# Optimization experiments

Measured on AMD Instinct MI355X. Metric: run time of the kernel, lower is better.

The kernel has to match this reference:

```python
import jax, jax.numpy as jnp
import numpy as np

B, N, C = 32, 512, 768
H = 12
D = C // H
HID = 4 * C
EPS = 1e-5


def layer_norm(x, w, b):
    mu = jnp.mean(x, axis=-1, keepdims=True)
    var = jnp.mean(jnp.square(x - mu), axis=-1, keepdims=True)
    return (x - mu) * jax.lax.rsqrt(var + EPS) * w + b


def setup_inputs() -> dict:
    key = jax.random.key(0)
    ks = jax.random.split(key, 8)
    s_in = 1.0 / np.sqrt(C)
    s_hid = 1.0 / np.sqrt(HID)
    return {
        "x": jax.random.normal(ks[0], (B, N, C), dtype=jnp.float32),
        "ln1_w": jnp.ones((C,), jnp.float32),
        "ln1_b": jnp.zeros((C,), jnp.float32),
        "qkv_w": jax.random.normal(ks[1], (3 * C, C), jnp.float32) * s_in,
        "proj_w": jax.random.normal(ks[2], (C, C), jnp.float32) * s_in,
        "proj_b": jnp.zeros((C,), jnp.float32),
        "ln2_w": jnp.ones((C,), jnp.float32),
        "ln2_b": jnp.zeros((C,), jnp.float32),
        "fc1_w": jax.random.normal(ks[3], (HID, C), jnp.float32) * s_in,
        "fc1_b": jnp.zeros((HID,), jnp.float32),
        "fc2_w": jax.random.normal(ks[4], (C, HID), jnp.float32) * s_hid,
        "fc2_b": jnp.zeros((C,), jnp.float32),
    }


def reference(x, ln1_w, ln1_b, qkv_w, proj_w, proj_b, ln2_w, ln2_b, fc1_w, fc1_b, fc2_w, fc2_b):
    scale = D ** (-0.5)
    # --- attention on norm1(x) ---
    h = layer_norm(x, ln1_w, ln1_b)                       # [B,N,C]
    qkv = jnp.einsum('bnc,fc->bnf', h, qkv_w)             # [B,N,3C] (no bias)
    qkv = qkv.reshape(B, N, 3, H, D).transpose(2, 0, 3, 1, 4)  # [3,B,H,N,D]
    q, k, v = qkv[0], qkv[1], qkv[2]
    attn = jnp.einsum('bhnd,bhmd->bhnm', q, k) * scale    # [B,H,N,N]
    attn = jax.nn.softmax(attn, axis=-1)
    o = jnp.einsum('bhnm,bhmd->bhnd', attn, v)            # [B,H,N,D]
    o = o.transpose(0, 2, 1, 3).reshape(B, N, C)
    o = jnp.einsum('bnc,oc->bno', o, proj_w) + proj_b
    # --- Block quirk: x = attn_out + drop_path(attn_out) == 2*attn_out (eval) ---
    x = o + o
    # --- MLP residual ---
    h2 = layer_norm(x, ln2_w, ln2_b)
    h2 = jnp.einsum('bnc,hc->bnh', h2, fc1_w) + fc1_b
    h2 = jax.nn.gelu(h2, approximate=False)
    h2 = jnp.einsum('bnh,oh->bno', h2, fc2_w) + fc2_b
    return x + h2
```

## Files before the change

### kernel.cpp

```cpp
#include <hip/hip_runtime.h>

#define B_   32
#define N_   512
#define C_   768
#define H_   12
#define D_   64
#define HID_ 3072
#define BN_  (B_*N_)

typedef unsigned short u16;
typedef __attribute__((ext_vector_type(8))) short  short8;
typedef __attribute__((ext_vector_type(4))) float  float4v;

__device__ __forceinline__ u16 f32_to_bf16(float f) {
  unsigned u = __builtin_bit_cast(unsigned, f);
  u += 0x7fffu + ((u >> 16) & 1u);
  return (u16)(u >> 16);
}

__device__ __forceinline__ void load_lds16(const u16* g, u16* l) {
  __builtin_amdgcn_global_load_lds(
      (const __attribute__((address_space(1))) unsigned int*)g,
      (__attribute__((address_space(3))) unsigned int*)l,
      16, 0, 0);
}

__global__ void cast_kernel(const float* __restrict__ src, u16* __restrict__ dst, int n) {
  int i = blockIdx.x * 256 + threadIdx.x;
  if (i < n) dst[i] = f32_to_bf16(src[i]);
}

__global__ __launch_bounds__(256)
void ln_kernel(const float* __restrict__ x, const float* __restrict__ w,
               const float* __restrict__ bias, u16* __restrict__ out) {
  const int row = blockIdx.x;
  const int tid = threadIdx.x;
  const float* xr = x + (size_t)row * C_;
  float v0 = xr[tid], v1 = xr[tid + 256], v2 = xr[tid + 512];
  float s = v0 + v1 + v2;
  float q = v0*v0 + v1*v1 + v2*v2;
#pragma unroll
  for (int off = 1; off < 64; off <<= 1) { s += __shfl_xor(s, off); q += __shfl_xor(q, off); }
  __shared__ float red[8];
  int wave = tid >> 6, lane = tid & 63;
  if (lane == 0) { red[wave] = s; red[4 + wave] = q; }
  __syncthreads();
  s = red[0] + red[1] + red[2] + red[3];
  q = red[4] + red[5] + red[6] + red[7];
  float mean = s * (1.0f / C_);
  float var  = q * (1.0f / C_) - mean * mean;
  float rstd = rsqrtf(var + 1e-5f);
  u16* orow = out + (size_t)row * C_;
  orow[tid]       = f32_to_bf16((v0 - mean) * rstd * w[tid]       + bias[tid]);
  orow[tid + 256] = f32_to_bf16((v1 - mean) * rstd * w[tid + 256] + bias[tid + 256]);
  orow[tid + 512] = f32_to_bf16((v2 - mean) * rstd * w[tid + 512] + bias[tid + 512]);
}

template <int EPI>
__device__ __forceinline__ void gemm_core(const u16* __restrict__ A, const u16* __restrict__ W,
                                          int N, int K,
                                          const float* __restrict__ bias,
                                          const float* __restrict__ resid,
                                          u16* __restrict__ out_bf, float* __restrict__ out_f) {
  __shared__ alignas(16) u16 As[128 * 64];
  __shared__ alignas(16) u16 Ws[128 * 64];
  const int tid  = threadIdx.x;
  const int wave = tid >> 6;
  const int lane = tid & 63;
  const int quad = lane >> 4;
  const int l15  = lane & 15;

  const int nx    = gridDim.x;
  const int lin   = blockIdx.y * nx + blockIdx.x;
  const int total = nx * gridDim.y;
  const int v     = (lin & 7) * (total >> 3) + (lin >> 3);
  const int m0 = (v / nx) << 7;
  const int n0 = (v % nx) << 7;

  const int wm = (wave >> 1) * 64;
  const int wn = (wave & 1) * 64;

  float4v acc[4][4];
#pragma unroll
  for (int i = 0; i < 4; i++)
#pragma unroll
    for (int j = 0; j < 4; j++) acc[i][j] = (float4v){0.f, 0.f, 0.f, 0.f};

  const int c0   = wave * 4;
  const int srow = lane >> 3;
  const int gcol = ((lane & 7) ^ srow) * 8;
  const u16* Ag[4];
  const u16* Wg[4];
#pragma unroll
  for (int j = 0; j < 4; j++) {
    const int row = (c0 + j) * 8 + srow;
    Ag[j] = A + (size_t)(m0 + row) * K + gcol;
    Wg[j] = W + (size_t)(n0 + row) * K + gcol;
  }

  for (int k0 = 0; k0 < K; k0 += 64) {
    __syncthreads();
#pragma unroll
    for (int j = 0; j < 4; j++) load_lds16(Ag[j] + k0, &As[(c0 + j) * 512]);
#pragma unroll
    for (int j = 0; j < 4; j++) load_lds16(Wg[j] + k0, &Ws[(c0 + j) * 512]);
    __syncthreads();

    short8 af[4][2], bf[4][2];
#pragma unroll
    for (int mi = 0; mi < 4; mi++)
#pragma unroll
      for (int ks = 0; ks < 2; ks++) {
        const int swz = ((ks * 4 + quad) ^ (l15 & 7)) * 8;
        af[mi][ks] = *(const short8*)&As[(wm + mi * 16 + l15) * 64 + swz];
        bf[mi][ks] = *(const short8*)&Ws[(wn + mi * 16 + l15) * 64 + swz];
      }
#pragma unroll
    for (int ks = 0; ks < 2; ks++)
#pragma unroll
      for (int mi = 0; mi < 4; mi++)
#pragma unroll
        for (int ni = 0; ni < 4; ni++)
          acc[mi][ni] = __builtin_amdgcn_mfma_f32_16x16x32_bf16(af[mi][ks], bf[ni][ks], acc[mi][ni], 0, 0, 0);
  }

#pragma unroll
  for (int mi = 0; mi < 4; mi++) {
#pragma unroll
    for (int r = 0; r < 4; r++) {
      const int row = m0 + wm + mi * 16 + quad * 4 + r;
#pragma unroll
      for (int ni = 0; ni < 4; ni++) {
        const int col = n0 + wn + ni * 16 + l15;
        float v2 = acc[mi][ni][r];
        if (EPI == 0) {
          out_bf[(size_t)row * N + col] = f32_to_bf16(v2);
        } else if (EPI == 1) {
          v2 += bias[col];
          v2 = 0.5f * v2 * (1.0f + erff(v2 * 0.70710678118654752f));
          out_bf[(size_t)row * N + col] = f32_to_bf16(v2);
        } else if (EPI == 2) {
          out_f[(size_t)row * N + col] = 2.0f * (v2 + bias[col]);
        } else {
          out_f[(size_t)row * N + col] = v2 + bias[col] + resid[(size_t)row * N + col];
        }
      }
    }
  }
}

__global__ __launch_bounds__(256, 3)
void gemm_qkv(const u16* __restrict__ A, const u16* __restrict__ W, int N, int K,
              u16* __restrict__ out_bf) {
  gemm_core<0>(A, W, N, K, nullptr, nullptr, out_bf, nullptr);
}
__global__ __launch_bounds__(256, 3)
void gemm_proj2x(const u16* __restrict__ A, const u16* __restrict__ W, int N, int K,
                 const float* __restrict__ bias, float* __restrict__ out_f) {
  gemm_core<2>(A, W, N, K, bias, nullptr, nullptr, out_f);
}
__global__ __launch_bounds__(256, 3)
void gemm_fc1gelu(const u16* __restrict__ A, const u16* __restrict__ W, int N, int K,
                  const float* __restrict__ bias, u16* __restrict__ out_bf) {
  gemm_core<1>(A, W, N, K, bias, nullptr, out_bf, nullptr);
}
__global__ __launch_bounds__(256, 3)
void gemm_fc2res(const u16* __restrict__ A, const u16* __restrict__ W, int N, int K,
                 const float* __restrict__ bias, const float* __restrict__ resid,
                 float* __restrict__ out_f) {
  gemm_core<3>(A, W, N, K, bias, resid, nullptr, out_f);
}

__global__ __launch_bounds__(256)
void attn_kernel(const u16* __restrict__ qkv, u16* __restrict__ o) {
  __shared__ alignas(16) u16 Ks[64 * 64];
  __shared__ alignas(16) u16 Vt[64 * 64];
  __shared__ alignas(16) u16 Ps[4][16 * 64];
  const int tid  = threadIdx.x;
  const int wave = tid >> 6, lane = tid & 63;
  const int quad = lane >> 4, l15 = lane & 15;
  const int qt = blockIdx.x, h = blockIdx.y, b = blockIdx.z;
  const size_t rs3 = 3 * C_;

  const int qrow = b * N_ + qt * 64 + wave * 16 + l15;
  const u16* qp = qkv + (size_t)qrow * rs3 + h * D_ + quad * 8;
  const short8 qf0 = *(const short8*)qp;
  const short8 qf1 = *(const short8*)(qp + 32);

  float m[4], l[4];
  float4v oacc[4];
#pragma unroll
  for (int r = 0; r < 4; r++) { m[r] = -1e30f; l[r] = 0.f; }
#pragma unroll
  for (int ni = 0; ni < 4; ni++) oacc[ni] = (float4v){0.f, 0.f, 0.f, 0.f};

  const int vkey = tid >> 2, vdg = tid & 3;

  for (int kt = 0; kt < 8; ++kt) {
    __syncthreads();
    {
      int c0 = wave * 2, c1 = c0 + 1;
      int kr0 = c0 * 8 + (lane >> 3), kr1 = c1 * 8 + (lane >> 3);
      int kc = (lane & 7) * 8;
      const u16* kg = qkv + (size_t)(b * N_ + kt * 64) * rs3 + C_ + h * D_;
      load_lds16(kg + (size_t)kr0 * rs3 + kc, &Ks[c0 * 512]);
      load_lds16(kg + (size_t)kr1 * rs3 + kc, &Ks[c1 * 512]);
    }
    {
      const u16* vg = qkv + (size_t)(b * N_ + kt * 64 + vkey) * rs3 + 2 * C_ + h * D_ + vdg * 16;
      short8 v0 = *(const short8*)vg;
      short8 v1 = *(const short8*)(vg + 8);
#pragma unroll
      for (int j = 0; j < 8; j++) Vt[(vdg * 16 + j) * 64 + vkey] = (u16)v0[j];
#pragma unroll
      for (int j = 0; j < 8; j++) Vt[(vdg * 16 + 8 + j) * 64 + vkey] = (u16)v1[j];
    }
    __syncthreads();

    float4v s[4];
#pragma unroll
    for (int ni = 0; ni < 4; ni++) {
      s[ni] = (float4v){0.f, 0.f, 0.f, 0.f};
      short8 kf0 = *(const short8*)&Ks[(ni * 16 + l15) * 64 + quad * 8];
      short8 kf1 = *(const short8*)&Ks[(ni * 16 + l15) * 64 + 32 + quad * 8];
      s[ni] = __builtin_amdgcn_mfma_f32_16x16x32_bf16(qf0, kf0, s[ni], 0, 0, 0);
      s[ni] = __builtin_amdgcn_mfma_f32_16x16x32_bf16(qf1, kf1, s[ni], 0, 0, 0);
    }

    float mt[4];
#pragma unroll
    for (int r = 0; r < 4; r++)
      mt[r] = 0.125f * fmaxf(fmaxf(s[0][r], s[1][r]), fmaxf(s[2][r], s[3][r]));
#pragma unroll
    for (int off = 1; off < 16; off <<= 1)
#pragma unroll
      for (int r = 0; r < 4; r++) mt[r] = fmaxf(mt[r], __shfl_xor(mt[r], off));

    float alpha[4], mnew[4], rsum[4];
#pragma unroll
    for (int r = 0; r < 4; r++) {
      mnew[r] = fmaxf(m[r], mt[r]);
      alpha[r] = __expf(m[r] - mnew[r]);
      rsum[r] = 0.f;
    }
#pragma unroll
    for (int ni = 0; ni < 4; ni++)
#pragma unroll
      for (int r = 0; r < 4; r++) {
        float p = __expf(s[ni][r] * 0.125f - mnew[r]);
        rsum[r] += p;
        Ps[wave][(quad * 4 + r) * 64 + ni * 16 + l15] = f32_to_bf16(p);
      }
#pragma unroll
    for (int off = 1; off < 16; off <<= 1)
#pragma unroll
      for (int r = 0; r < 4; r++) rsum[r] += __shfl_xor(rsum[r], off);
#pragma unroll
    for (int r = 0; r < 4; r++) { l[r] = l[r] * alpha[r] + rsum[r]; m[r] = mnew[r]; }
#pragma unroll
    for (int ni = 0; ni < 4; ni++)
#pragma unroll
      for (int r = 0; r < 4; r++) oacc[ni][r] *= alpha[r];

    __syncthreads();

#pragma unroll
    for (int ks = 0; ks < 2; ks++) {
      short8 pf = *(const short8*)&Ps[wave][l15 * 64 + ks * 32 + quad * 8];
#pragma unroll
      for (int ni = 0; ni < 4; ni++) {
        short8 vf = *(const short8*)&Vt[(ni * 16 + l15) * 64 + ks * 32 + quad * 8];
        oacc[ni] = __builtin_amdgcn_mfma_f32_16x16x32_bf16(pf, vf, oacc[ni], 0, 0, 0);
      }
    }
  }

#pragma unroll
  for (int ni = 0; ni < 4; ni++)
#pragma unroll
    for (int r = 0; r < 4; r++) {
      int row = b * N_ + qt * 64 + wave * 16 + quad * 4 + r;
      int col = h * D_ + ni * 16 + l15;
      o[(size_t)row * C_ + col] = f32_to_bf16(oacc[ni][r] / l[r]);
    }
}

extern "C" void kernel_launch(void* const* d_in, const int* in_sizes, int n_in,
                              void* d_out, int out_size, void* d_ws, size_t ws_size,
                              hipStream_t stream) {
  const float* x      = (const float*)d_in[0];
  const float* ln1_w  = (const float*)d_in[1];
  const float* ln1_b  = (const float*)d_in[2];
  const float* qkv_w  = (const float*)d_in[3];
  const float* proj_w = (const float*)d_in[4];
  const float* proj_b = (const float*)d_in[5];
  const float* ln2_w  = (const float*)d_in[6];
  const float* ln2_b  = (const float*)d_in[7];
  const float* fc1_w  = (const float*)d_in[8];
  const float* fc1_b  = (const float*)d_in[9];
  const float* fc2_w  = (const float*)d_in[10];
  const float* fc2_b  = (const float*)d_in[11];
  float* out = (float*)d_out;

  char* ws = (char*)d_ws;
  size_t off = 0;
  auto alloc = [&](size_t bytes) { void* p = ws + off; off += (bytes + 255) & ~255ull; return p; };
  u16* wqkv  = (u16*)alloc((size_t)3 * C_ * C_ * 2);
  u16* wproj = (u16*)alloc((size_t)C_ * C_ * 2);
  u16* wfc1  = (u16*)alloc((size_t)HID_ * C_ * 2);
  u16* wfc2  = (u16*)alloc((size_t)C_ * HID_ * 2);
  u16* regionA = (u16*)alloc((size_t)BN_ * HID_ * 2);
  float* xnew  = (float*)alloc((size_t)BN_ * C_ * 4);
  u16* h2      = (u16*)alloc((size_t)BN_ * C_ * 2);

  u16* hbuf = regionA;
  u16* qkvb = regionA + (size_t)BN_ * C_;
  u16* obuf = regionA;
  u16* act  = regionA;

  cast_kernel<<<dim3(3 * C_ * C_ / 256), 256, 0, stream>>>(qkv_w, wqkv, 3 * C_ * C_);
  cast_kernel<<<dim3(C_ * C_ / 256), 256, 0, stream>>>(proj_w, wproj, C_ * C_);
  cast_kernel<<<dim3(HID_ * C_ / 256), 256, 0, stream>>>(fc1_w, wfc1, HID_ * C_);
  cast_kernel<<<dim3(HID_ * C_ / 256), 256, 0, stream>>>(fc2_w, wfc2, C_ * HID_);

  ln_kernel<<<dim3(BN_), 256, 0, stream>>>(x, ln1_w, ln1_b, hbuf);

  gemm_qkv<<<dim3(3 * C_ / 128, BN_ / 128), 256, 0, stream>>>(hbuf, wqkv, 3 * C_, C_, qkvb);

  attn_kernel<<<dim3(N_ / 64, H_, B_), 256, 0, stream>>>(qkvb, obuf);

  gemm_proj2x<<<dim3(C_ / 128, BN_ / 128), 256, 0, stream>>>(obuf, wproj, C_, C_, proj_b, xnew);

  ln_kernel<<<dim3(BN_), 256, 0, stream>>>(xnew, ln2_w, ln2_b, h2);

  gemm_fc1gelu<<<dim3(HID_ / 128, BN_ / 128), 256, 0, stream>>>(h2, wfc1, HID_, C_, fc1_b, act);

  gemm_fc2res<<<dim3(C_ / 128, BN_ / 128), 256, 0, stream>>>(act, wfc2, C_, HID_, fc2_b, xnew, out);
}
```

Baseline: 573.7 us.

## Write V transposed from QKV GEMM and read K/V directly in attention

The QKV GEMM epilogue now writes the V columns in a per-head transposed [B,H,D,N] layout into a reused workspace buffer. The attention kernel drops the shared-memory staging of K and V and loads MFMA fragments straight from global memory, which also removes the block-wide barriers. The per-wave P tile gets an XOR swizzle against bank conflicts, and the final division becomes a reciprocal multiply. In exchange, the V stores in the GEMM are scattered and uncoalesced, and every wave now reads K/V from global memory or cache without reuse through LDS.

```diff
diff --git a/kernel.cpp b/kernel.cpp
--- a/kernel.cpp
+++ b/kernel.cpp
@@ -61,7 +61,8 @@
                                           int N, int K,
                                           const float* __restrict__ bias,
                                           const float* __restrict__ resid,
-                                          u16* __restrict__ out_bf, float* __restrict__ out_f) {
+                                          u16* __restrict__ out_bf, float* __restrict__ out_f,
+                                          u16* __restrict__ vt_out) {
   __shared__ alignas(16) u16 As[128 * 64];
   __shared__ alignas(16) u16 Ws[128 * 64];
   const int tid  = threadIdx.x;
@@ -134,7 +135,14 @@
         const int col = n0 + wn + ni * 16 + l15;
         float v2 = acc[mi][ni][r];
         if (EPI == 0) {
-          out_bf[(size_t)row * N + col] = f32_to_bf16(v2);
+          if (col < 2 * C_) {
+            out_bf[(size_t)row * N + col] = f32_to_bf16(v2);
+          } else {
+            const int voff = col - 2 * C_;
+            const int hh = voff >> 6, dd = voff & 63;
+            const int bb = row >> 9, nn = row & 511;
+            vt_out[((size_t)(bb * H_ + hh) * D_ + dd) * N_ + nn] = f32_to_bf16(v2);
+          }
         } else if (EPI == 1) {
           v2 += bias[col];
           v2 = 0.5f * v2 * (1.0f + erff(v2 * 0.70710678118654752f));
@@ -151,42 +159,45 @@
 
 __global__ __launch_bounds__(256, 3)
 void gemm_qkv(const u16* __restrict__ A, const u16* __restrict__ W, int N, int K,
-              u16* __restrict__ out_bf) {
-  gemm_core<0>(A, W, N, K, nullptr, nullptr, out_bf, nullptr);
+              u16* __restrict__ out_bf, u16* __restrict__ vt_out) {
+  gemm_core<0>(A, W, N, K, nullptr, nullptr, out_bf, nullptr, vt_out);
 }
 __global__ __launch_bounds__(256, 3)
 void gemm_proj2x(const u16* __restrict__ A, const u16* __restrict__ W, int N, int K,
                  const float* __restrict__ bias, float* __restrict__ out_f) {
-  gemm_core<2>(A, W, N, K, bias, nullptr, nullptr, out_f);
+  gemm_core<2>(A, W, N, K, bias, nullptr, nullptr, out_f, nullptr);
 }
 __global__ __launch_bounds__(256, 3)
 void gemm_fc1gelu(const u16* __restrict__ A, const u16* __restrict__ W, int N, int K,
                   const float* __restrict__ bias, u16* __restrict__ out_bf) {
-  gemm_core<1>(A, W, N, K, bias, nullptr, out_bf, nullptr);
+  gemm_core<1>(A, W, N, K, bias, nullptr, out_bf, nullptr, nullptr);
 }
 __global__ __launch_bounds__(256, 3)
 void gemm_fc2res(const u16* __restrict__ A, const u16* __restrict__ W, int N, int K,
                  const float* __restrict__ bias, const float* __restrict__ resid,
                  float* __restrict__ out_f) {
-  gemm_core<3>(A, W, N, K, bias, resid, nullptr, out_f);
+  gemm_core<3>(A, W, N, K, bias, resid, nullptr, out_f, nullptr);
 }
 
 __global__ __launch_bounds__(256)
-void attn_kernel(const u16* __restrict__ qkv, u16* __restrict__ o) {
-  __shared__ alignas(16) u16 Ks[64 * 64];
-  __shared__ alignas(16) u16 Vt[64 * 64];
+void attn_kernel(const u16* __restrict__ qkv, const u16* __restrict__ vt,
+                 u16* __restrict__ o) {
   __shared__ alignas(16) u16 Ps[4][16 * 64];
   const int tid  = threadIdx.x;
   const int wave = tid >> 6, lane = tid & 63;
   const int quad = lane >> 4, l15 = lane & 15;
   const int qt = blockIdx.x, h = blockIdx.y, b = blockIdx.z;
   const size_t rs3 = 3 * C_;
+  u16* myPs = Ps[wave];
 
   const int qrow = b * N_ + qt * 64 + wave * 16 + l15;
   const u16* qp = qkv + (size_t)qrow * rs3 + h * D_ + quad * 8;
   const short8 qf0 = *(const short8*)qp;
   const short8 qf1 = *(const short8*)(qp + 32);
 
+  const u16* kbase = qkv + (size_t)(b * N_) * rs3 + C_ + h * D_ + quad * 8;
+  const u16* vbase = vt + (size_t)(b * H_ + h) * D_ * N_ + quad * 8;
+
   float m[4], l[4];
   float4v oacc[4];
 #pragma unroll
@@ -194,35 +205,14 @@
 #pragma unroll
   for (int ni = 0; ni < 4; ni++) oacc[ni] = (float4v){0.f, 0.f, 0.f, 0.f};
 
-  const int vkey = tid >> 2, vdg = tid & 3;
-
   for (int kt = 0; kt < 8; ++kt) {
-    __syncthreads();
-    {
-      int c0 = wave * 2, c1 = c0 + 1;
-      int kr0 = c0 * 8 + (lane >> 3), kr1 = c1 * 8 + (lane >> 3);
-      int kc = (lane & 7) * 8;
-      const u16* kg = qkv + (size_t)(b * N_ + kt * 64) * rs3 + C_ + h * D_;
-      load_lds16(kg + (size_t)kr0 * rs3 + kc, &Ks[c0 * 512]);
-      load_lds16(kg + (size_t)kr1 * rs3 + kc, &Ks[c1 * 512]);
-    }
-    {
-      const u16* vg = qkv + (size_t)(b * N_ + kt * 64 + vkey) * rs3 + 2 * C_ + h * D_ + vdg * 16;
-      short8 v0 = *(const short8*)vg;
-      short8 v1 = *(const short8*)(vg + 8);
-#pragma unroll
-      for (int j = 0; j < 8; j++) Vt[(vdg * 16 + j) * 64 + vkey] = (u16)v0[j];
-#pragma unroll
-      for (int j = 0; j < 8; j++) Vt[(vdg * 16 + 8 + j) * 64 + vkey] = (u16)v1[j];
-    }
-    __syncthreads();
-
     float4v s[4];
 #pragma unroll
     for (int ni = 0; ni < 4; ni++) {
+      const u16* kr = kbase + (size_t)(kt * 64 + ni * 16 + l15) * rs3;
+      short8 kf0 = *(const short8*)kr;
+      short8 kf1 = *(const short8*)(kr + 32);
       s[ni] = (float4v){0.f, 0.f, 0.f, 0.f};
-      short8 kf0 = *(const short8*)&Ks[(ni * 16 + l15) * 64 + quad * 8];
-      short8 kf1 = *(const short8*)&Ks[(ni * 16 + l15) * 64 + 32 + quad * 8];
       s[ni] = __builtin_amdgcn_mfma_f32_16x16x32_bf16(qf0, kf0, s[ni], 0, 0, 0);
       s[ni] = __builtin_amdgcn_mfma_f32_16x16x32_bf16(qf1, kf1, s[ni], 0, 0, 0);
     }
@@ -249,7 +239,9 @@
       for (int r = 0; r < 4; r++) {
         float p = __expf(s[ni][r] * 0.125f - mnew[r]);
         rsum[r] += p;
-        Ps[wave][(quad * 4 + r) * 64 + ni * 16 + l15] = f32_to_bf16(p);
+        const int prow = quad * 4 + r;
+        const int g = (ni * 2 + (l15 >> 3)) ^ (prow & 7);
+        myPs[prow * 64 + g * 8 + (l15 & 7)] = f32_to_bf16(p);
       }
 #pragma unroll
     for (int off = 1; off < 16; off <<= 1)
@@ -262,26 +254,29 @@
 #pragma unroll
       for (int r = 0; r < 4; r++) oacc[ni][r] *= alpha[r];
 
-    __syncthreads();
-
 #pragma unroll
     for (int ks = 0; ks < 2; ks++) {
-      short8 pf = *(const short8*)&Ps[wave][l15 * 64 + ks * 32 + quad * 8];
+      const int g = (ks * 4 + quad) ^ (l15 & 7);
+      short8 pf = *(const short8*)&myPs[l15 * 64 + g * 8];
 #pragma unroll
       for (int ni = 0; ni < 4; ni++) {
-        short8 vf = *(const short8*)&Vt[(ni * 16 + l15) * 64 + ks * 32 + quad * 8];
+        const u16* vr = vbase + (size_t)(ni * 16 + l15) * N_ + kt * 64 + ks * 32;
+        short8 vf = *(const short8*)vr;
         oacc[ni] = __builtin_amdgcn_mfma_f32_16x16x32_bf16(pf, vf, oacc[ni], 0, 0, 0);
       }
     }
   }
 
+  float inv[4];
+#pragma unroll
+  for (int r = 0; r < 4; r++) inv[r] = 1.0f / l[r];
 #pragma unroll
   for (int ni = 0; ni < 4; ni++)
 #pragma unroll
     for (int r = 0; r < 4; r++) {
       int row = b * N_ + qt * 64 + wave * 16 + quad * 4 + r;
       int col = h * D_ + ni * 16 + l15;
-      o[(size_t)row * C_ + col] = f32_to_bf16(oacc[ni][r] / l[r]);
+      o[(size_t)row * C_ + col] = f32_to_bf16(oacc[ni][r] * inv[r]);
     }
 }
 
@@ -317,6 +312,7 @@
   u16* qkvb = regionA + (size_t)BN_ * C_;
   u16* obuf = regionA;
   u16* act  = regionA;
+  u16* vtbuf = (u16*)xnew;
 
   cast_kernel<<<dim3(3 * C_ * C_ / 256), 256, 0, stream>>>(qkv_w, wqkv, 3 * C_ * C_);
   cast_kernel<<<dim3(C_ * C_ / 256), 256, 0, stream>>>(proj_w, wproj, C_ * C_);
@@ -325,9 +321,9 @@
 
   ln_kernel<<<dim3(BN_), 256, 0, stream>>>(x, ln1_w, ln1_b, hbuf);
 
-  gemm_qkv<<<dim3(3 * C_ / 128, BN_ / 128), 256, 0, stream>>>(hbuf, wqkv, 3 * C_, C_, qkvb);
-
-  attn_kernel<<<dim3(N_ / 64, H_, B_), 256, 0, stream>>>(qkvb, obuf);
+  gemm_qkv<<<dim3(3 * C_ / 128, BN_ / 128), 256, 0, stream>>>(hbuf, wqkv, 3 * C_, C_, qkvb, vtbuf);
+
+  attn_kernel<<<dim3(N_ / 64, H_, B_), 256, 0, stream>>>(qkvb, vtbuf, obuf);
 
   gemm_proj2x<<<dim3(C_ / 128, BN_ / 128), 256, 0, stream>>>(obuf, wproj, C_, C_, proj_b, xnew);
 
```

After: 666.1 us. +16.1%, slower.

## Pre-transpose V and process two query tiles per attention block with swizzled LDS

Applied to the files above, without the earlier changes.

Adds a separate kernel that transposes V into a per-head [D,N] buffer, reusing the xnew scratch region, so the attention kernel can stream both K and V into LDS with async global-to-LDS loads instead of a scalar transposing scatter. Each attention block now handles 128 queries, two 64-row subtiles per wave, so every K/V tile loaded is reused twice, and the grid is linearised with the query tile as the slow index. K, V and P in LDS use an XOR swizzle to avoid bank conflicts, and the barrier between the softmax and the PV product is removed because each wave owns its P buffer. This costs an extra kernel launch plus a round trip of V through memory, and roughly doubles the register state per thread.

```diff
diff --git a/kernel.cpp b/kernel.cpp
--- a/kernel.cpp
+++ b/kernel.cpp
@@ -56,6 +56,28 @@
   orow[tid + 512] = f32_to_bf16((v2 - mean) * rstd * w[tid + 512] + bias[tid + 512]);
 }
 
+__global__ __launch_bounds__(256)
+void transpose_v(const u16* __restrict__ qkv, u16* __restrict__ vt) {
+  __shared__ alignas(16) u16 T[64 * 72];
+  const int nt = blockIdx.x, bh = blockIdx.y;
+  const int b = bh / H_, h = bh % H_;
+  const int tid = threadIdx.x;
+  const size_t rs3 = 3 * C_;
+  const int r = tid >> 2, dc = (tid & 3) * 16;
+  const u16* src = qkv + (size_t)(b * N_ + nt * 64 + r) * rs3 + 2 * C_ + h * D_ + dc;
+  short8 a0 = *(const short8*)src;
+  short8 a1 = *(const short8*)(src + 8);
+#pragma unroll
+  for (int j = 0; j < 8; j++) T[(dc + j) * 72 + r] = (u16)a0[j];
+#pragma unroll
+  for (int j = 0; j < 8; j++) T[(dc + 8 + j) * 72 + r] = (u16)a1[j];
+  __syncthreads();
+  const int d = tid >> 2, nc = (tid & 3) * 16;
+  u16* dst = vt + ((size_t)(b * H_ + h) * D_ + d) * N_ + nt * 64 + nc;
+  *(short8*)dst       = *(const short8*)&T[d * 72 + nc];
+  *(short8*)(dst + 8) = *(const short8*)&T[d * 72 + nc + 8];
+}
+
 template <int EPI>
 __device__ __forceinline__ void gemm_core(const u16* __restrict__ A, const u16* __restrict__ W,
                                           int N, int K,
@@ -172,117 +194,137 @@
 }
 
 __global__ __launch_bounds__(256)
-void attn_kernel(const u16* __restrict__ qkv, u16* __restrict__ o) {
+void attn_kernel(const u16* __restrict__ qkv, const u16* __restrict__ vt,
+                 u16* __restrict__ o) {
   __shared__ alignas(16) u16 Ks[64 * 64];
-  __shared__ alignas(16) u16 Vt[64 * 64];
-  __shared__ alignas(16) u16 Ps[4][16 * 64];
+  __shared__ alignas(16) u16 Vs[64 * 64];
+  __shared__ alignas(16) u16 Ps[8][16 * 64];
   const int tid  = threadIdx.x;
   const int wave = tid >> 6, lane = tid & 63;
   const int quad = lane >> 4, l15 = lane & 15;
-  const int qt = blockIdx.x, h = blockIdx.y, b = blockIdx.z;
+  const int lin = blockIdx.x;
+  const int bh = lin % 384, qt = lin / 384;
+  const int b = bh / H_, h = bh % H_;
   const size_t rs3 = 3 * C_;
 
-  const int qrow = b * N_ + qt * 64 + wave * 16 + l15;
-  const u16* qp = qkv + (size_t)qrow * rs3 + h * D_ + quad * 8;
-  const short8 qf0 = *(const short8*)qp;
-  const short8 qf1 = *(const short8*)(qp + 32);
-
-  float m[4], l[4];
-  float4v oacc[4];
-#pragma unroll
-  for (int r = 0; r < 4; r++) { m[r] = -1e30f; l[r] = 0.f; }
-#pragma unroll
-  for (int ni = 0; ni < 4; ni++) oacc[ni] = (float4v){0.f, 0.f, 0.f, 0.f};
-
-  const int vkey = tid >> 2, vdg = tid & 3;
+  short8 qf[2][2];
+#pragma unroll
+  for (int st = 0; st < 2; st++) {
+    const int qrow = b * N_ + qt * 128 + st * 64 + wave * 16 + l15;
+    const u16* qp = qkv + (size_t)qrow * rs3 + h * D_ + quad * 8;
+    qf[st][0] = *(const short8*)qp;
+    qf[st][1] = *(const short8*)(qp + 32);
+  }
+
+  const int srow = lane >> 3;
+  const int gcol = ((lane & 7) ^ srow) * 8;
+  const int ch0 = wave * 2, ch1 = wave * 2 + 1;
+  const u16* kg0 = qkv + (size_t)(b * N_ + ch0 * 8 + srow) * rs3 + C_ + h * D_ + gcol;
+  const u16* kg1 = qkv + (size_t)(b * N_ + ch1 * 8 + srow) * rs3 + C_ + h * D_ + gcol;
+  const u16* vg0 = vt + ((size_t)bh * D_ + ch0 * 8 + srow) * N_ + gcol;
+  const u16* vg1 = vt + ((size_t)bh * D_ + ch1 * 8 + srow) * N_ + gcol;
+
+  float m[2][4], l[2][4];
+  float4v oacc[2][4];
+#pragma unroll
+  for (int st = 0; st < 2; st++)
+#pragma unroll
+    for (int r = 0; r < 4; r++) { m[st][r] = -1e30f; l[st][r] = 0.f; }
+#pragma unroll
+  for (int st = 0; st < 2; st++)
+#pragma unroll
+    for (int ni = 0; ni < 4; ni++) oacc[st][ni] = (float4v){0.f, 0.f, 0.f, 0.f};
 
   for (int kt = 0; kt < 8; ++kt) {
     __syncthreads();
-    {
-      int c0 = wave * 2, c1 = c0 + 1;
-      int kr0 = c0 * 8 + (lane >> 3), kr1 = c1 * 8 + (lane >> 3);
-      int kc = (lane & 7) * 8;
-      const u16* kg = qkv + (size_t)(b * N_ + kt * 64) * rs3 + C_ + h * D_;
-      load_lds16(kg + (size_t)kr0 * rs3 + kc, &Ks[c0 * 512]);
-      load_lds16(kg + (size_t)kr1 * rs3 + kc, &Ks[c1 * 512]);
+    load_lds16(kg0 + (size_t)(kt * 64) * rs3, &Ks[ch0 * 512]);
+    load_lds16(kg1 + (size_t)(kt * 64) * rs3, &Ks[ch1 * 512]);
+    load_lds16(vg0 + kt * 64, &Vs[ch0 * 512]);
+    load_lds16(vg1 + kt * 64, &Vs[ch1 * 512]);
+    __syncthreads();
+
+    short8 kf[4][2];
+#pragma unroll
+    for (int ni = 0; ni < 4; ni++)
+#pragma unroll
+      for (int ks = 0; ks < 2; ks++)
+        kf[ni][ks] = *(const short8*)&Ks[(ni * 16 + l15) * 64 + ((ks * 4 + quad) ^ (l15 & 7)) * 8];
+
+#pragma unroll
+    for (int st = 0; st < 2; st++) {
+      u16* myPs = Ps[wave * 2 + st];
+      float4v s[4];
+#pragma unroll
+      for (int ni = 0; ni < 4; ni++) {
+        s[ni] = (float4v){0.f, 0.f, 0.f, 0.f};
+        s[ni] = __builtin_amdgcn_mfma_f32_16x16x32_bf16(qf[st][0], kf[ni][0], s[ni], 0, 0, 0);
+        s[ni] = __builtin_amdgcn_mfma_f32_16x16x32_bf16(qf[st][1], kf[ni][1], s[ni], 0, 0, 0);
+      }
+
+      float mt[4];
+#pragma unroll
+      for (int r = 0; r < 4; r++)
+        mt[r] = 0.125f * fmaxf(fmaxf(s[0][r], s[1][r]), fmaxf(s[2][r], s[3][r]));
+#pragma unroll
+      for (int off = 1; off < 16; off <<= 1)
+#pragma unroll
+        for (int r = 0; r < 4; r++) mt[r] = fmaxf(mt[r], __shfl_xor(mt[r], off));
+
+      float alpha[4], mnew[4], rsum[4];
+#pragma unroll
+      for (int r = 0; r < 4; r++) {
+        mnew[r] = fmaxf(m[st][r], mt[r]);
+        alpha[r] = __expf(m[st][r] - mnew[r]);
+        rsum[r] = 0.f;
+      }
+#pragma unroll
+      for (int ni = 0; ni < 4; ni++)
+#pragma unroll
+        for (int r = 0; r < 4; r++) {
+          float p = __expf(s[ni][r] * 0.125f - mnew[r]);
+          rsum[r] += p;
+          const int prow = quad * 4 + r;
+          const int g = (ni * 2 + (l15 >> 3)) ^ (prow & 7);
+          myPs[prow * 64 + g * 8 + (l15 & 7)] = f32_to_bf16(p);
+        }
+#pragma unroll
+      for (int off = 1; off < 16; off <<= 1)
+#pragma unroll
+        for (int r = 0; r < 4; r++) rsum[r] += __shfl_xor(rsum[r], off);
+#pragma unroll
+      for (int r = 0; r < 4; r++) { l[st][r] = l[st][r] * alpha[r] + rsum[r]; m[st][r] = mnew[r]; }
+#pragma unroll
+      for (int ni = 0; ni < 4; ni++)
+#pragma unroll
+        for (int r = 0; r < 4; r++) oacc[st][ni][r] *= alpha[r];
+
+#pragma unroll
+      for (int ks = 0; ks < 2; ks++) {
+        const int g = (ks * 4 + quad) ^ (l15 & 7);
+        short8 pf = *(const short8*)&myPs[l15 * 64 + g * 8];
+#pragma unroll
+        for (int ni = 0; ni < 4; ni++) {
+          short8 vf = *(const short8*)&Vs[(ni * 16 + l15) * 64 + ((ks * 4 + quad) ^ (l15 & 7)) * 8];
+          oacc[st][ni] = __builtin_amdgcn_mfma_f32_16x16x32_bf16(pf, vf, oacc[st][ni], 0, 0, 0);
+        }
+      }
     }
-    {
-      const u16* vg = qkv + (size_t)(b * N_ + kt * 64 + vkey) * rs3 + 2 * C_ + h * D_ + vdg * 16;
-      short8 v0 = *(const short8*)vg;
-      short8 v1 = *(const short8*)(vg + 8);
-#pragma unroll
-      for (int j = 0; j < 8; j++) Vt[(vdg * 16 + j) * 64 + vkey] = (u16)v0[j];
-#pragma unroll
-      for (int j = 0; j < 8; j++) Vt[(vdg * 16 + 8 + j) * 64 + vkey] = (u16)v1[j];
-    }
-    __syncthreads();
-
-    float4v s[4];
-#pragma unroll
-    for (int ni = 0; ni < 4; ni++) {
-      s[ni] = (float4v){0.f, 0.f, 0.f, 0.f};
-      short8 kf0 = *(const short8*)&Ks[(ni * 16 + l15) * 64 + quad * 8];
-      short8 kf1 = *(const short8*)&Ks[(ni * 16 + l15) * 64 + 32 + quad * 8];
-      s[ni] = __builtin_amdgcn_mfma_f32_16x16x32_bf16(qf0, kf0, s[ni], 0, 0, 0);
-      s[ni] = __builtin_amdgcn_mfma_f32_16x16x32_bf16(qf1, kf1, s[ni], 0, 0, 0);
-    }
-
-    float mt[4];
-#pragma unroll
-    for (int r = 0; r < 4; r++)
-      mt[r] = 0.125f * fmaxf(fmaxf(s[0][r], s[1][r]), fmaxf(s[2][r], s[3][r]));
-#pragma unroll
-    for (int off = 1; off < 16; off <<= 1)
-#pragma unroll
-      for (int r = 0; r < 4; r++) mt[r] = fmaxf(mt[r], __shfl_xor(mt[r], off));
-
-    float alpha[4], mnew[4], rsum[4];
-#pragma unroll
-    for (int r = 0; r < 4; r++) {
-      mnew[r] = fmaxf(m[r], mt[r]);
-      alpha[r] = __expf(m[r] - mnew[r]);
-      rsum[r] = 0.f;
-    }
+  }
+
+#pragma unroll
+  for (int st = 0; st < 2; st++) {
+    float inv[4];
+#pragma unroll
+    for (int r = 0; r < 4; r++) inv[r] = 1.0f / l[st][r];
 #pragma unroll
     for (int ni = 0; ni < 4; ni++)
 #pragma unroll
       for (int r = 0; r < 4; r++) {
-        float p = __expf(s[ni][r] * 0.125f - mnew[r]);
-        rsum[r] += p;
-        Ps[wave][(quad * 4 + r) * 64 + ni * 16 + l15] = f32_to_bf16(p);
-      }
-#pragma unroll
-    for (int off = 1; off < 16; off <<= 1)
-#pragma unroll
-      for (int r = 0; r < 4; r++) rsum[r] += __shfl_xor(rsum[r], off);
-#pragma unroll
-    for (int r = 0; r < 4; r++) { l[r] = l[r] * alpha[r] + rsum[r]; m[r] = mnew[r]; }
-#pragma unroll
-    for (int ni = 0; ni < 4; ni++)
-#pragma unroll
-      for (int r = 0; r < 4; r++) oacc[ni][r] *= alpha[r];
-
-    __syncthreads();
-
-#pragma unroll
-    for (int ks = 0; ks < 2; ks++) {
-      short8 pf = *(const short8*)&Ps[wave][l15 * 64 + ks * 32 + quad * 8];
-#pragma unroll
-      for (int ni = 0; ni < 4; ni++) {
-        short8 vf = *(const short8*)&Vt[(ni * 16 + l15) * 64 + ks * 32 + quad * 8];
-        oacc[ni] = __builtin_amdgcn_mfma_f32_16x16x32_bf16(pf, vf, oacc[ni], 0, 0, 0);
-      }
-    }
-  }
-
-#pragma unroll
-  for (int ni = 0; ni < 4; ni++)
-#pragma unroll
-    for (int r = 0; r < 4; r++) {
-      int row = b * N_ + qt * 64 + wave * 16 + quad * 4 + r;
-      int col = h * D_ + ni * 16 + l15;
-      o[(size_t)row * C_ + col] = f32_to_bf16(oacc[ni][r] / l[r]);
-    }
+        int row = b * N_ + qt * 128 + st * 64 + wave * 16 + quad * 4 + r;
+        int col = h * D_ + ni * 16 + l15;
+        o[(size_t)row * C_ + col] = f32_to_bf16(oacc[st][ni][r] * inv[r]);
+      }
+  }
 }
 
 extern "C" void kernel_launch(void* const* d_in, const int* in_sizes, int n_in,
@@ -317,6 +359,7 @@
   u16* qkvb = regionA + (size_t)BN_ * C_;
   u16* obuf = regionA;
   u16* act  = regionA;
+  u16* vtbuf = (u16*)xnew;
 
   cast_kernel<<<dim3(3 * C_ * C_ / 256), 256, 0, stream>>>(qkv_w, wqkv, 3 * C_ * C_);
   cast_kernel<<<dim3(C_ * C_ / 256), 256, 0, stream>>>(proj_w, wproj, C_ * C_);
@@ -327,7 +370,9 @@
 
   gemm_qkv<<<dim3(3 * C_ / 128, BN_ / 128), 256, 0, stream>>>(hbuf, wqkv, 3 * C_, C_, qkvb);
 
-  attn_kernel<<<dim3(N_ / 64, H_, B_), 256, 0, stream>>>(qkvb, obuf);
+  transpose_v<<<dim3(N_ / 64, B_ * H_), 256, 0, stream>>>(qkvb, vtbuf);
+
+  attn_kernel<<<dim3((N_ / 128) * B_ * H_), 256, 0, stream>>>(qkvb, vtbuf, obuf);
 
   gemm_proj2x<<<dim3(C_ / 128, BN_ / 128), 256, 0, stream>>>(obuf, wproj, C_, C_, proj_b, xnew);
 
```

After: 555.8 us. 3.1% less time.
